# Optimization experiments

Hardware: AMD Instinct MI355X
Metric: run time of the kernel (lower is better)

## Reference

```python
import jax, jax.numpy as jnp
import numpy as np

B, S, D_IN, D_HEAD = 4, 4096, 1024, 64

def setup_inputs() -> dict:
    key = jax.random.key(0)
    k1, k2, k3, k4 = jax.random.split(key, 4)
    scale = 0.02
    return {
        "input_vectors": jax.random.normal(k1, (B, S, D_IN), dtype=jnp.float32),
        "Wq": jax.random.normal(k2, (D_IN, D_HEAD), dtype=jnp.float32) * scale,
        "Wk": jax.random.normal(k3, (D_IN, D_HEAD), dtype=jnp.float32) * scale,
        "Wv": jax.random.normal(k4, (D_IN, D_HEAD), dtype=jnp.float32) * scale,
    }

def reference(input_vectors, Wq, Wk, Wv):
    # QKV projections (Linear with no bias): [B,S,d_in] @ [d_in,d_head]
    q = input_vectors @ Wq  # [B,S,H]
    k = input_vectors @ Wk
    v = input_vectors @ Wv
    n = input_vectors.shape[1]
    # causal attention scores: [B,S,S]
    scores = jnp.einsum('bqh,bkh->bqk', q, k)
    causal = jnp.tril(jnp.ones((n, n), dtype=bool))  # True = keep
    scores = jnp.where(causal, scores, -jnp.inf)
    scale = k.shape[-1] ** -0.5
    attn = jax.nn.softmax(scores * scale, axis=-1)
    return jnp.einsum('bqk,bkh->bqh', attn, v)
```

## Files before the change

kernel.cpp:

```cpp
#include <hip/hip_runtime.h>
#include <stdint.h>

#define SEQ   4096
#define DIN   1024

typedef __attribute__((ext_vector_type(8))) short bf16x8;
typedef __attribute__((ext_vector_type(4))) float floatx4;
typedef __attribute__((ext_vector_type(4))) unsigned short ushortx4;

#if __has_builtin(__builtin_amdgcn_exp2f)
#define EXP2(x) __builtin_amdgcn_exp2f(x)
#else
#define EXP2(x) exp2f(x)
#endif

__device__ __forceinline__ unsigned short f2bf(float f) {
    union { float f; unsigned int u; } v; v.f = f;
    unsigned int u = v.u + 0x7fffu + ((v.u >> 16) & 1u);
    return (unsigned short)(u >> 16);
}
__device__ __forceinline__ float bf2f(unsigned short h) {
    union { unsigned int u; float f; } v; v.u = ((unsigned int)h) << 16;
    return v.f;
}
__device__ __forceinline__ float uasf(unsigned int u) {
    union { unsigned int u; float f; } v; v.u = u; return v.f;
}
__device__ __forceinline__ unsigned int fasu(float f) {
    union { float f; unsigned int u; } v; v.f = f; return v.u;
}
__device__ __forceinline__ float dpp_xor1(float x) {
    return uasf((unsigned)__builtin_amdgcn_mov_dpp((int)fasu(x), 0xB1, 0xF, 0xF, true));
}
__device__ __forceinline__ float dpp_xor2(float x) {
    return uasf((unsigned)__builtin_amdgcn_mov_dpp((int)fasu(x), 0x4E, 0xF, 0xF, true));
}

__global__ void wt_prep(const float* __restrict__ Wq, const float* __restrict__ Wk,
                        const float* __restrict__ Wv, unsigned short* __restrict__ WT) {
    int idx = blockIdx.x * 256 + threadIdx.x;
    int k   = idx & 1023;
    int n   = (idx >> 10) & 63;
    int mat = idx >> 16;
    const float* W = (mat == 0) ? Wq : ((mat == 1) ? Wk : Wv);
    WT[idx] = f2bf(W[k * 64 + n]);
}

#define QSCALE 0.18033688011112042f
__launch_bounds__(512, 2)
__global__ void proj_qkv(const float* __restrict__ X, const unsigned short* __restrict__ WT,
                         unsigned short* __restrict__ qb, unsigned short* __restrict__ kb,
                         unsigned short* __restrict__ vb) {
    __shared__ __align__(16) float          X0[64 * 64], X1[64 * 64];
    __shared__ __align__(16) unsigned short W0[192 * 64], W1[192 * 64];
    const int tid = threadIdx.x;
    const int wave = tid >> 6, lane = tid & 63;
    const int quad = lane >> 4, l16 = lane & 15;
    const int strip = wave >> 1;
    const int cg = wave & 1;
    const int row0 = blockIdx.x * 64;
    const int m = strip * 16 + l16;

    floatx4 acc[6];
#pragma unroll
    for (int i = 0; i < 6; i++) acc[i] = (floatx4){0.f, 0.f, 0.f, 0.f};

    int xu[2], xr[2], xc[2], wu[3], wr[3], wc[3];
#pragma unroll
    for (int i = 0; i < 2; i++) {
        xu[i] = i * 512 + tid; xr[i] = xu[i] >> 4; xc[i] = (xu[i] & 15) ^ (xr[i] & 15);
    }
#pragma unroll
    for (int i = 0; i < 3; i++) {
        wu[i] = i * 512 + tid; wr[i] = wu[i] >> 3; wc[i] = (wu[i] & 7) ^ (wr[i] & 7);
    }
    floatx4 xpre[2], wpre[3];
    auto issue = [&](int k0) {
#pragma unroll
        for (int i = 0; i < 2; i++)
            xpre[i] = *(const floatx4*)(X + (size_t)(row0 + xr[i]) * DIN + k0 + xc[i] * 4);
#pragma unroll
        for (int i = 0; i < 3; i++)
            wpre[i] = *(const floatx4*)(WT + (size_t)wr[i] * 1024 + k0 + wc[i] * 8);
    };

    issue(0);
    for (int kc = 0; kc < 16; kc++) {
        float*          Xd = (kc & 1) ? X1 : X0;
        unsigned short* Wd = (kc & 1) ? W1 : W0;
#pragma unroll
        for (int i = 0; i < 2; i++) *(floatx4*)&Xd[xu[i] * 4] = xpre[i];
#pragma unroll
        for (int i = 0; i < 3; i++) *(floatx4*)&Wd[wu[i] * 8] = wpre[i];
        if (kc < 15) issue((kc + 1) * 64);
        __syncthreads();

        bf16x8 af[2];
#pragma unroll
        for (int ks = 0; ks < 2; ks++) {
            floatx4 x0 = *(const floatx4*)&Xd[m * 64 + ((ks * 8 + quad * 2 + 0) ^ (m & 15)) * 4];
            floatx4 x1 = *(const floatx4*)&Xd[m * 64 + ((ks * 8 + quad * 2 + 1) ^ (m & 15)) * 4];
#pragma unroll
            for (int j = 0; j < 4; j++) {
                af[ks][j]     = (short)f2bf(x0[j]);
                af[ks][j + 4] = (short)f2bf(x1[j]);
            }
        }
#pragma unroll
        for (int i = 0; i < 6; i++) {
            const int nrow = (cg * 6 + i) * 16 + l16;
#pragma unroll
            for (int ks = 0; ks < 2; ks++) {
                const int c = ks * 4 + quad;
                bf16x8 bfrag = *(const bf16x8*)&Wd[nrow * 64 + (c ^ (nrow & 7)) * 8];
                acc[i] = __builtin_amdgcn_mfma_f32_16x16x32_bf16(af[ks], bfrag, acc[i], 0, 0, 0);
            }
        }
    }
#pragma unroll
    for (int i = 0; i < 6; i++) {
        const int nt = cg * 6 + i;
        const int mat = nt >> 2;
        const int col = (nt & 3) * 16 + l16;
#pragma unroll
        for (int r = 0; r < 4; r++) {
            const int orow = row0 + strip * 16 + quad * 4 + r;
            float v = acc[i][r];
            if (mat == 0) {
                qb[(size_t)orow * 64 + col] = f2bf(v * QSCALE);
            } else if (mat == 1) {
                kb[(size_t)orow * 64 + col] = f2bf(v);
            } else {
                int b = orow >> 12, sq = orow & 4095;
                vb[((size_t)b * 64 + col) * SEQ + sq] = f2bf(v);
            }
        }
    }
}

__launch_bounds__(256, 4)
__global__ void attn(const unsigned short* __restrict__ qb, const unsigned short* __restrict__ kb,
                     const unsigned short* __restrict__ vb, unsigned short* __restrict__ opart,
                     float* __restrict__ lpart) {
    __shared__ __align__(16) unsigned short Kl[64 * 64];
    __shared__ __align__(16) unsigned short Vl[64 * 64];
    __shared__ __align__(16) unsigned short Pl[4][16 * 72];

    const int bid = blockIdx.x;
    const int qt = 63 - (bid >> 4);
    const int batch = (bid >> 2) & 3;
    const int s = bid & 3;
    const int q0 = qt * 64;
    const int T = qt + 1;
    const int lo = (T * s) >> 2, hi = (T * (s + 1)) >> 2;

    const int tid = threadIdx.x;
    const int wave = tid >> 6, lane = tid & 63;
    const int quad = lane >> 4, l16 = lane & 15;

    const unsigned short* qr = qb + (size_t)(batch * SEQ + q0 + wave * 16 + l16) * 64;
    bf16x8 qa0 = *(const bf16x8*)(qr + quad * 8);
    bf16x8 qa1 = *(const bf16x8*)(qr + 32 + quad * 8);

    floatx4 o[4];
#pragma unroll
    for (int i = 0; i < 4; i++) o[i] = (floatx4){0.f, 0.f, 0.f, 0.f};
    float lsum = 0.f;

    const unsigned short* kbase = kb + (size_t)batch * SEQ * 64;
    const unsigned short* vbase = vb + (size_t)batch * 64 * SEQ;
    unsigned short* P = &Pl[wave][0];

    int ku[2], kr[2], kc_[2], vu[2], vd[2], vc[2];
#pragma unroll
    for (int i = 0; i < 2; i++) {
        ku[i] = i * 256 + tid; kr[i] = ku[i] >> 3; kc_[i] = (ku[i] & 7) ^ (kr[i] & 7);
        vu[i] = i * 256 + tid; vd[i] = vu[i] >> 3; vc[i] = (vu[i] & 7) ^ (vd[i] & 7);
    }
    floatx4 kpre[2], vpre[2];
    auto issue = [&](int k0) {
#pragma unroll
        for (int i = 0; i < 2; i++)
            kpre[i] = *(const floatx4*)(kbase + (size_t)(k0 + kr[i]) * 64 + kc_[i] * 8);
#pragma unroll
        for (int i = 0; i < 2; i++)
            vpre[i] = *(const floatx4*)(vbase + (size_t)vd[i] * SEQ + k0 + vc[i] * 8);
    };

    if (lo < hi) issue(lo * 64);
    for (int kt = lo; kt < hi; kt++) {
        __syncthreads();
#pragma unroll
        for (int i = 0; i < 2; i++) *(floatx4*)&Kl[ku[i] * 8] = kpre[i];
#pragma unroll
        for (int i = 0; i < 2; i++) *(floatx4*)&Vl[vu[i] * 8] = vpre[i];
        if (kt + 1 < hi) issue((kt + 1) * 64);
        __syncthreads();

        const int k0 = kt * 64;
        floatx4 sc[4];
#pragma unroll
        for (int nt = 0; nt < 4; nt++) {
            sc[nt] = (floatx4){0.f, 0.f, 0.f, 0.f};
            const int key = nt * 16 + l16;
#pragma unroll
            for (int ks = 0; ks < 2; ks++) {
                const int c = ks * 4 + quad;
                bf16x8 bk = *(const bf16x8*)&Kl[key * 64 + (c ^ (key & 7)) * 8];
                sc[nt] = __builtin_amdgcn_mfma_f32_16x16x32_bf16(
                    ks == 0 ? qa0 : qa1, bk, sc[nt], 0, 0, 0);
            }
        }
        if (kt == T - 1) {
#pragma unroll
            for (int nt = 0; nt < 4; nt++) {
                const int col = k0 + nt * 16 + l16;
#pragma unroll
                for (int r = 0; r < 4; r++) {
                    const int rowg = q0 + wave * 16 + quad * 4 + r;
                    if (col > rowg) sc[nt][r] = -1e30f;
                }
            }
        }
#pragma unroll
        for (int nt = 0; nt < 4; nt++) {
            float v0 = EXP2(sc[nt][0]), v1 = EXP2(sc[nt][1]);
            float v2 = EXP2(sc[nt][2]), v3 = EXP2(sc[nt][3]);
            float t0 = dpp_xor2(v0), t1 = dpp_xor2(v1), t2 = dpp_xor2(v2), t3 = dpp_xor2(v3);
            if (lane & 2) { v0 = t2; v1 = t3; } else { v2 = t0; v3 = t1; }
            t0 = dpp_xor1(v0); t1 = dpp_xor1(v1); t2 = dpp_xor1(v2); t3 = dpp_xor1(v3);
            if (lane & 1) { v0 = t1; v2 = t3; } else { v1 = t0; v3 = t2; }
            unsigned int u0 = fasu(v0) & 0xffff0000u, u1 = fasu(v1) & 0xffff0000u;
            unsigned int u2 = fasu(v2) & 0xffff0000u, u3 = fasu(v3) & 0xffff0000u;
            lsum += (uasf(u0) + uasf(u1)) + (uasf(u2) + uasf(u3));
            uint2 w;
            w.x = (u0 >> 16) | u1;
            w.y = (u2 >> 16) | u3;
            const int prow = quad * 4 + (lane & 3);
            const int pcol = nt * 16 + (l16 >> 2) * 4;
            *(uint2*)&P[prow * 72 + pcol] = w;
        }
#pragma unroll
        for (int ks = 0; ks < 2; ks++) {
            bf16x8 pa = *(const bf16x8*)&P[l16 * 72 + ks * 32 + quad * 8];
#pragma unroll
            for (int nt = 0; nt < 4; nt++) {
                const int d = nt * 16 + l16;
                bf16x8 bv = *(const bf16x8*)&Vl[d * 64 + ((ks * 4 + quad) ^ (d & 7)) * 8];
                o[nt] = __builtin_amdgcn_mfma_f32_16x16x32_bf16(pa, bv, o[nt], 0, 0, 0);
            }
        }
    }

    unsigned short* ob = opart + (size_t)s * (4 * SEQ * 64)
                       + (size_t)(batch * SEQ + q0 + wave * 16) * 64;
    float* lb = lpart + (size_t)s * (4 * SEQ) + (batch * SEQ + q0 + wave * 16);
    float l = lsum;
    l += __shfl_xor(l, 4);
    l += __shfl_xor(l, 8);
#pragma unroll
    for (int nt = 0; nt < 4; nt++)
#pragma unroll
        for (int r = 0; r < 4; r++)
            ob[(quad * 4 + r) * 64 + nt * 16 + l16] = f2bf(o[nt][r]);
    if ((l16 >> 2) == 0) lb[quad * 4 + (lane & 3)] = l;
}

__global__ void merge(const unsigned short* __restrict__ opart, const float* __restrict__ lpart,
                      float* __restrict__ out) {
    int idx = blockIdx.x * 256 + threadIdx.x;
    int row = idx >> 4, c4 = idx & 15;
    float l = lpart[row] + lpart[4 * SEQ + row] + lpart[8 * SEQ + row] + lpart[12 * SEQ + row];
    float inv = 1.f / l;
    floatx4 acc = (floatx4){0.f, 0.f, 0.f, 0.f};
#pragma unroll
    for (int s = 0; s < 4; s++) {
        ushortx4 u = *(const ushortx4*)(opart + (size_t)s * (4 * SEQ * 64)
                                        + (size_t)row * 64 + c4 * 4);
#pragma unroll
        for (int j = 0; j < 4; j++) acc[j] += bf2f(u[j]);
    }
    acc *= inv;
    *(floatx4*)(out + (size_t)row * 64 + c4 * 4) = acc;
}

extern "C" void kernel_launch(void* const* d_in, const int* in_sizes, int n_in,
                              void* d_out, int out_size, void* d_ws, size_t ws_size,
                              hipStream_t stream) {
    const float* X  = (const float*)d_in[0];
    const float* Wq = (const float*)d_in[1];
    const float* Wk = (const float*)d_in[2];
    const float* Wv = (const float*)d_in[3];
    float* out = (float*)d_out;
    char* ws = (char*)d_ws;
    unsigned short* WT    = (unsigned short*)(ws + 0);
    unsigned short* qb    = (unsigned short*)(ws + 393216);
    unsigned short* kb    = (unsigned short*)(ws + 2490368);
    unsigned short* vb    = (unsigned short*)(ws + 4587520);
    unsigned short* opart = (unsigned short*)(ws + 6684672);
    float*          lpart = (float*)(ws + 15073280);

    hipLaunchKernelGGL(wt_prep,  dim3(768),  dim3(256), 0, stream, Wq, Wk, Wv, WT);
    hipLaunchKernelGGL(proj_qkv, dim3(256),  dim3(512), 0, stream, X, WT, qb, kb, vb);
    hipLaunchKernelGGL(attn,     dim3(1024), dim3(256), 0, stream, qb, kb, vb, opart, lpart);
    hipLaunchKernelGGL(merge,    dim3(1024), dim3(256), 0, stream, opart, lpart, out);
}
```

Baseline: 135.0 us.

## Fuse split-K merge into attention via atomic counter and widen blocks

The attention kernel now processes 128-row query tiles with 8 waves per block, and blocks are ordered to pair long and short causal tiles. Per-wave causal skipping and masking replace the old last-tile mask. The separate merge kernel is removed: the last split to finish for a tile, detected by an atomic counter, combines the partial outputs and normalises them. The projection kernel also moves to 1024 threads with 3 output tiles per wave. This trades one launch and the merge pass for atomics, a memset, more registers per block and a possible tail imbalance.

New measurement: 161.0 us. 1.19x slower.

```diff
diff --git a/kernel.cpp b/kernel.cpp
--- a/kernel.cpp
+++ b/kernel.cpp
@@ -47,7 +47,7 @@
 }
 
 #define QSCALE 0.18033688011112042f
-__launch_bounds__(512, 2)
+__launch_bounds__(1024, 4)
 __global__ void proj_qkv(const float* __restrict__ X, const unsigned short* __restrict__ WT,
                          unsigned short* __restrict__ qb, unsigned short* __restrict__ kb,
                          unsigned short* __restrict__ vb) {
@@ -56,42 +56,34 @@
     const int tid = threadIdx.x;
     const int wave = tid >> 6, lane = tid & 63;
     const int quad = lane >> 4, l16 = lane & 15;
-    const int strip = wave >> 1;
-    const int cg = wave & 1;
+    const int strip = wave >> 2;
+    const int cg = wave & 3;
     const int row0 = blockIdx.x * 64;
     const int m = strip * 16 + l16;
 
-    floatx4 acc[6];
-#pragma unroll
-    for (int i = 0; i < 6; i++) acc[i] = (floatx4){0.f, 0.f, 0.f, 0.f};
-
-    int xu[2], xr[2], xc[2], wu[3], wr[3], wc[3];
-#pragma unroll
-    for (int i = 0; i < 2; i++) {
-        xu[i] = i * 512 + tid; xr[i] = xu[i] >> 4; xc[i] = (xu[i] & 15) ^ (xr[i] & 15);
-    }
-#pragma unroll
-    for (int i = 0; i < 3; i++) {
-        wu[i] = i * 512 + tid; wr[i] = wu[i] >> 3; wc[i] = (wu[i] & 7) ^ (wr[i] & 7);
-    }
-    floatx4 xpre[2], wpre[3];
+    floatx4 acc[3];
+#pragma unroll
+    for (int i = 0; i < 3; i++) acc[i] = (floatx4){0.f, 0.f, 0.f, 0.f};
+
+    const int xu = tid, xr = xu >> 4, xc = (xu & 15) ^ (xr & 15);
+    const int wu0 = tid, wr0 = wu0 >> 3, wc0 = (wu0 & 7) ^ (wr0 & 7);
+    const int wu1 = 1024 + tid, wr1 = wu1 >> 3, wc1 = (wu1 & 7) ^ (wr1 & 7);
+    const bool w2 = (tid < 512);
+
+    floatx4 xpre, wpre0, wpre1;
     auto issue = [&](int k0) {
-#pragma unroll
-        for (int i = 0; i < 2; i++)
-            xpre[i] = *(const floatx4*)(X + (size_t)(row0 + xr[i]) * DIN + k0 + xc[i] * 4);
-#pragma unroll
-        for (int i = 0; i < 3; i++)
-            wpre[i] = *(const floatx4*)(WT + (size_t)wr[i] * 1024 + k0 + wc[i] * 8);
+        xpre = *(const floatx4*)(X + (size_t)(row0 + xr) * DIN + k0 + xc * 4);
+        wpre0 = *(const floatx4*)(WT + (size_t)wr0 * 1024 + k0 + wc0 * 8);
+        if (w2) wpre1 = *(const floatx4*)(WT + (size_t)wr1 * 1024 + k0 + wc1 * 8);
     };
 
     issue(0);
     for (int kc = 0; kc < 16; kc++) {
         float*          Xd = (kc & 1) ? X1 : X0;
         unsigned short* Wd = (kc & 1) ? W1 : W0;
-#pragma unroll
-        for (int i = 0; i < 2; i++) *(floatx4*)&Xd[xu[i] * 4] = xpre[i];
-#pragma unroll
-        for (int i = 0; i < 3; i++) *(floatx4*)&Wd[wu[i] * 8] = wpre[i];
+        *(floatx4*)&Xd[xu * 4] = xpre;
+        *(floatx4*)&Wd[wu0 * 8] = wpre0;
+        if (w2) *(floatx4*)&Wd[wu1 * 8] = wpre1;
         if (kc < 15) issue((kc + 1) * 64);
         __syncthreads();
 
@@ -107,8 +99,8 @@
             }
         }
 #pragma unroll
-        for (int i = 0; i < 6; i++) {
-            const int nrow = (cg * 6 + i) * 16 + l16;
+        for (int i = 0; i < 3; i++) {
+            const int nrow = (cg * 3 + i) * 16 + l16;
 #pragma unroll
             for (int ks = 0; ks < 2; ks++) {
                 const int c = ks * 4 + quad;
@@ -116,10 +108,11 @@
                 acc[i] = __builtin_amdgcn_mfma_f32_16x16x32_bf16(af[ks], bfrag, acc[i], 0, 0, 0);
             }
         }
-    }
-#pragma unroll
-    for (int i = 0; i < 6; i++) {
-        const int nt = cg * 6 + i;
+        __syncthreads();
+    }
+#pragma unroll
+    for (int i = 0; i < 3; i++) {
+        const int nt = cg * 3 + i;
         const int mat = nt >> 2;
         const int col = (nt & 3) * 16 + l16;
 #pragma unroll
@@ -138,27 +131,30 @@
     }
 }
 
-__launch_bounds__(256, 4)
+__launch_bounds__(512, 4)
 __global__ void attn(const unsigned short* __restrict__ qb, const unsigned short* __restrict__ kb,
                      const unsigned short* __restrict__ vb, unsigned short* __restrict__ opart,
-                     float* __restrict__ lpart) {
+                     float* __restrict__ lpart, unsigned int* __restrict__ cnt,
+                     float* __restrict__ out) {
     __shared__ __align__(16) unsigned short Kl[64 * 64];
     __shared__ __align__(16) unsigned short Vl[64 * 64];
-    __shared__ __align__(16) unsigned short Pl[4][16 * 72];
+    __shared__ __align__(16) unsigned short Pl[8][16 * 72];
+    __shared__ int lastflag;
 
     const int bid = blockIdx.x;
-    const int qt = 63 - (bid >> 4);
+    const int qt = (bid < 256) ? (31 - (bid >> 4)) : ((bid - 256) >> 4);
     const int batch = (bid >> 2) & 3;
     const int s = bid & 3;
-    const int q0 = qt * 64;
-    const int T = qt + 1;
+    const int q0 = qt * 128;
+    const int T = 2 * qt + 2;
     const int lo = (T * s) >> 2, hi = (T * (s + 1)) >> 2;
 
     const int tid = threadIdx.x;
     const int wave = tid >> 6, lane = tid & 63;
     const int quad = lane >> 4, l16 = lane & 15;
-
-    const unsigned short* qr = qb + (size_t)(batch * SEQ + q0 + wave * 16 + l16) * 64;
+    const int rbase = q0 + wave * 16;
+
+    const unsigned short* qr = qb + (size_t)(batch * SEQ + rbase + l16) * 64;
     bf16x8 qa0 = *(const bf16x8*)(qr + quad * 8);
     bf16x8 qa1 = *(const bf16x8*)(qr + 32 + quad * 8);
 
@@ -171,33 +167,25 @@
     const unsigned short* vbase = vb + (size_t)batch * 64 * SEQ;
     unsigned short* P = &Pl[wave][0];
 
-    int ku[2], kr[2], kc_[2], vu[2], vd[2], vc[2];
-#pragma unroll
-    for (int i = 0; i < 2; i++) {
-        ku[i] = i * 256 + tid; kr[i] = ku[i] >> 3; kc_[i] = (ku[i] & 7) ^ (kr[i] & 7);
-        vu[i] = i * 256 + tid; vd[i] = vu[i] >> 3; vc[i] = (vu[i] & 7) ^ (vd[i] & 7);
-    }
-    floatx4 kpre[2], vpre[2];
+    const int kr = tid >> 3, kc_ = (tid & 7) ^ (kr & 7);
+    const int vd = tid >> 3, vc = (tid & 7) ^ (vd & 7);
+    floatx4 kpre, vpre;
     auto issue = [&](int k0) {
-#pragma unroll
-        for (int i = 0; i < 2; i++)
-            kpre[i] = *(const floatx4*)(kbase + (size_t)(k0 + kr[i]) * 64 + kc_[i] * 8);
-#pragma unroll
-        for (int i = 0; i < 2; i++)
-            vpre[i] = *(const floatx4*)(vbase + (size_t)vd[i] * SEQ + k0 + vc[i] * 8);
+        kpre = *(const floatx4*)(kbase + (size_t)(k0 + kr) * 64 + kc_ * 8);
+        vpre = *(const floatx4*)(vbase + (size_t)vd * SEQ + k0 + vc * 8);
     };
 
     if (lo < hi) issue(lo * 64);
     for (int kt = lo; kt < hi; kt++) {
         __syncthreads();
-#pragma unroll
-        for (int i = 0; i < 2; i++) *(floatx4*)&Kl[ku[i] * 8] = kpre[i];
-#pragma unroll
-        for (int i = 0; i < 2; i++) *(floatx4*)&Vl[vu[i] * 8] = vpre[i];
+        *(floatx4*)&Kl[tid * 8] = kpre;
+        *(floatx4*)&Vl[tid * 8] = vpre;
         if (kt + 1 < hi) issue((kt + 1) * 64);
         __syncthreads();
 
         const int k0 = kt * 64;
+        if (k0 > rbase + 15) continue;
+
         floatx4 sc[4];
 #pragma unroll
         for (int nt = 0; nt < 4; nt++) {
@@ -211,13 +199,13 @@
                     ks == 0 ? qa0 : qa1, bk, sc[nt], 0, 0, 0);
             }
         }
-        if (kt == T - 1) {
+        if (k0 + 63 > rbase) {
 #pragma unroll
             for (int nt = 0; nt < 4; nt++) {
                 const int col = k0 + nt * 16 + l16;
 #pragma unroll
                 for (int r = 0; r < 4; r++) {
-                    const int rowg = q0 + wave * 16 + quad * 4 + r;
+                    const int rowg = rbase + quad * 4 + r;
                     if (col > rowg) sc[nt][r] = -1e30f;
                 }
             }
@@ -253,8 +241,8 @@
     }
 
     unsigned short* ob = opart + (size_t)s * (4 * SEQ * 64)
-                       + (size_t)(batch * SEQ + q0 + wave * 16) * 64;
-    float* lb = lpart + (size_t)s * (4 * SEQ) + (batch * SEQ + q0 + wave * 16);
+                       + (size_t)(batch * SEQ + rbase) * 64;
+    float* lb = lpart + (size_t)s * (4 * SEQ) + (batch * SEQ + rbase);
     float l = lsum;
     l += __shfl_xor(l, 4);
     l += __shfl_xor(l, 8);
@@ -264,24 +252,33 @@
         for (int r = 0; r < 4; r++)
             ob[(quad * 4 + r) * 64 + nt * 16 + l16] = f2bf(o[nt][r]);
     if ((l16 >> 2) == 0) lb[quad * 4 + (lane & 3)] = l;
-}
-
-__global__ void merge(const unsigned short* __restrict__ opart, const float* __restrict__ lpart,
-                      float* __restrict__ out) {
-    int idx = blockIdx.x * 256 + threadIdx.x;
-    int row = idx >> 4, c4 = idx & 15;
-    float l = lpart[row] + lpart[4 * SEQ + row] + lpart[8 * SEQ + row] + lpart[12 * SEQ + row];
-    float inv = 1.f / l;
-    floatx4 acc = (floatx4){0.f, 0.f, 0.f, 0.f};
-#pragma unroll
-    for (int s = 0; s < 4; s++) {
-        ushortx4 u = *(const ushortx4*)(opart + (size_t)s * (4 * SEQ * 64)
-                                        + (size_t)row * 64 + c4 * 4);
-#pragma unroll
-        for (int j = 0; j < 4; j++) acc[j] += bf2f(u[j]);
-    }
-    acc *= inv;
-    *(floatx4*)(out + (size_t)row * 64 + c4 * 4) = acc;
+
+    __syncthreads();
+    if (tid == 0) {
+        __threadfence();
+        unsigned int old = __hip_atomic_fetch_add(&cnt[batch * 32 + qt], 1u,
+                                                  __ATOMIC_ACQ_REL, __HIP_MEMORY_SCOPE_AGENT);
+        lastflag = (old == 3u);
+    }
+    __syncthreads();
+    if (lastflag) {
+        for (int u = tid; u < 2048; u += 512) {
+            const int row = u >> 4, c4 = u & 15;
+            const int grow = batch * SEQ + q0 + row;
+            float lt = lpart[grow] + lpart[4 * SEQ + grow]
+                     + lpart[8 * SEQ + grow] + lpart[12 * SEQ + grow];
+            floatx4 acc = (floatx4){0.f, 0.f, 0.f, 0.f};
+#pragma unroll
+            for (int sp = 0; sp < 4; sp++) {
+                ushortx4 v = *(const ushortx4*)(opart + (size_t)sp * (4 * SEQ * 64)
+                                                + (size_t)grow * 64 + c4 * 4);
+#pragma unroll
+                for (int j = 0; j < 4; j++) acc[j] += bf2f(v[j]);
+            }
+            acc *= (1.f / lt);
+            *(floatx4*)(out + (size_t)grow * 64 + c4 * 4) = acc;
+        }
+    }
 }
 
 extern "C" void kernel_launch(void* const* d_in, const int* in_sizes, int n_in,
@@ -299,9 +296,11 @@
     unsigned short* vb    = (unsigned short*)(ws + 4587520);
     unsigned short* opart = (unsigned short*)(ws + 6684672);
     float*          lpart = (float*)(ws + 15073280);
-
-    hipLaunchKernelGGL(wt_prep,  dim3(768),  dim3(256), 0, stream, Wq, Wk, Wv, WT);
-    hipLaunchKernelGGL(proj_qkv, dim3(256),  dim3(512), 0, stream, X, WT, qb, kb, vb);
-    hipLaunchKernelGGL(attn,     dim3(1024), dim3(256), 0, stream, qb, kb, vb, opart, lpart);
-    hipLaunchKernelGGL(merge,    dim3(1024), dim3(256), 0, stream, opart, lpart, out);
-}
+    unsigned int*   cnt   = (unsigned int*)(ws + 15335424);
+
+    hipMemsetAsync(cnt, 0, 512, stream);
+    hipLaunchKernelGGL(wt_prep,  dim3(768), dim3(256),  0, stream, Wq, Wk, Wv, WT);
+    hipLaunchKernelGGL(proj_qkv, dim3(256), dim3(1024), 0, stream, X, WT, qb, kb, vb);
+    hipLaunchKernelGGL(attn,     dim3(512), dim3(512),  0, stream, qb, kb, vb,
+                       opart, lpart, cnt, out);
+}
```
